# Optimization experiments

Hardware: AMD Instinct MI355X
Metric: run time of the kernel (lower is better)

Reference implementation:

```python
import jax, jax.numpy as jnp
import numpy as np


def _gcn_norm(edge_index, n_nodes):
    # add self-loops, compute symmetric normalization coeffs (PyG gcn_norm)
    loop = jnp.arange(n_nodes, dtype=edge_index.dtype)
    src = jnp.concatenate([edge_index[0], loop])
    dst = jnp.concatenate([edge_index[1], loop])
    ones = jnp.ones(src.shape[0], dtype=jnp.float32)
    deg = jax.ops.segment_sum(ones, dst, num_segments=n_nodes)
    dinv = jnp.where(deg > 0, jax.lax.rsqrt(deg), 0.0)
    norm = dinv[src] * dinv[dst]  # (E + n_nodes,)
    return src, dst, norm


def _gcn_conv(x, W, b, src, dst, norm, n_nodes):
    h = x @ W                                   # (N, C_out) small dense GEMM first (PyG order)
    msg = h[src] * norm[:, None]                # gather + normalize
    out = jax.ops.segment_sum(msg, dst, num_segments=n_nodes)  # scatter-add aggregate
    return out + b


def setup_inputs() -> dict:
    key = jax.random.key(0)
    k1, k2, k3, k4, k5, k6 = jax.random.split(key, 6)
    n_nodes, n_edges = 100000, 1600000
    in_c, hid_c, out_c = 4, 32, 16
    x = jax.random.normal(k1, (n_nodes, in_c), dtype=jnp.float32)
    edge_index = jax.random.randint(k2, (2, n_edges), 0, n_nodes, dtype=jnp.int64)
    # Glorot init like PyG GCNConv.lin, zero bias
    s1 = float(np.sqrt(6.0 / (in_c + hid_c)))
    s2 = float(np.sqrt(6.0 / (hid_c + out_c)))
    W1 = jax.random.uniform(k3, (in_c, hid_c), jnp.float32, -s1, s1)
    b1 = jnp.zeros((hid_c,), jnp.float32)
    W2 = jax.random.uniform(k4, (hid_c, out_c), jnp.float32, -s2, s2)
    b2 = jnp.zeros((out_c,), jnp.float32)
    return {"x": x, "edge_index": edge_index, "W1": W1, "b1": b1, "W2": W2, "b2": b2}


def reference(x, edge_index, W1, b1, W2, b2):
    n_nodes = x.shape[0]
    src, dst, norm = _gcn_norm(edge_index, n_nodes)
    h = _gcn_conv(x, W1, b1, src, dst, norm, n_nodes)
    h = jax.nn.relu(h)
    # dropout is identity in eval mode
    z = _gcn_conv(h, W2, b2, src, dst, norm, n_nodes)
    return z
```

## Files before the change

kernel.cpp:

```cpp
#include <hip/hip_runtime.h>

constexpr int HID = 32;
constexpr int OUTC = 16;
constexpr int BIN = 256;
constexpr int BSH = 8;
constexpr int MAXNB = 1024;
constexpr int PTILE = 2048;

typedef int iv4 __attribute__((ext_vector_type(4)));

static __device__ __forceinline__ float4 ld4(const float* p) { return *(const float4*)p; }

__global__ void k_zero(int* __restrict__ bcnt) {
    bcnt[threadIdx.x] = 0;
}

__global__ void k_part(const int* __restrict__ src, const int* __restrict__ dst,
                       int* __restrict__ bcnt, int* __restrict__ elist,
                       int E, int nb, int capb) {
    __shared__ int hist[MAXNB];
    __shared__ int base[MAXNB];
    const int t = threadIdx.x;
    for (int i = t; i < nb; i += blockDim.x) hist[i] = 0;
    __syncthreads();
    const int E4 = E >> 2;
    int d[8], s[8], r[8];
    bool val[2];
#pragma unroll
    for (int q = 0; q < 2; ++q) {
        const int v = blockIdx.x * (PTILE / 4) + q * 256 + t;
        val[q] = (v < E4);
        if (val[q]) {
            iv4 d4 = __builtin_nontemporal_load(((const iv4*)dst) + v);
            iv4 s4 = __builtin_nontemporal_load(((const iv4*)src) + v);
            d[q*4+0] = d4.x; d[q*4+1] = d4.y; d[q*4+2] = d4.z; d[q*4+3] = d4.w;
            s[q*4+0] = s4.x; s[q*4+1] = s4.y; s[q*4+2] = s4.z; s[q*4+3] = s4.w;
#pragma unroll
            for (int k = q*4; k < q*4+4; ++k) r[k] = atomicAdd(&hist[d[k] >> BSH], 1);
        }
    }
    __syncthreads();
    for (int i = t; i < nb; i += blockDim.x) {
        int h = hist[i];
        base[i] = h ? atomicAdd(&bcnt[i], h) : 0;
    }
    __syncthreads();
#pragma unroll
    for (int q = 0; q < 2; ++q) {
        if (val[q]) {
#pragma unroll
            for (int k = q*4; k < q*4+4; ++k) {
                int bin = d[k] >> BSH;
                int pos = base[bin] + r[k];
                if (pos < capb) elist[(size_t)bin * capb + pos] = (s[k] << BSH) | (d[k] & (BIN-1));
            }
        }
    }
    if (blockIdx.x == 0 && t < (E & 3)) {
        int j = (E4 << 2) + t;
        int dd = dst[j], ss = src[j];
        int bin = dd >> BSH;
        int pos = atomicAdd(&bcnt[bin], 1);
        if (pos < capb) elist[(size_t)bin * capb + pos] = (ss << BSH) | (dd & (BIN-1));
    }
}

__global__ void k_fill3(const int* __restrict__ elist, const int* __restrict__ bcnt,
                        int* __restrict__ cursor, int* __restrict__ eidx,
                        const float* __restrict__ x, float* __restrict__ dinv,
                        float* __restrict__ y, int capb, int CAP, int N) {
    __shared__ int cnt[BIN];
    const int b = blockIdx.x;
    const int bin0 = b << BSH;
    const int tid = threadIdx.x;
    if (tid < BIN) cnt[tid] = 0;
    __syncthreads();
    const int ecnt = min(bcnt[b], capb);
    const int* lst = elist + (size_t)b * capb;
    for (int i0 = tid * 4; i0 + 3 < ecnt; i0 += blockDim.x * 4) {
        iv4 e = *(const iv4*)(lst + i0);
        int l0 = e.x & (BIN-1), s0 = (unsigned)e.x >> BSH;
        int l1 = e.y & (BIN-1), s1 = (unsigned)e.y >> BSH;
        int l2 = e.z & (BIN-1), s2 = (unsigned)e.z >> BSH;
        int l3 = e.w & (BIN-1), s3 = (unsigned)e.w >> BSH;
        int p0 = atomicAdd(&cnt[l0], 1);
        int p1 = atomicAdd(&cnt[l1], 1);
        int p2 = atomicAdd(&cnt[l2], 1);
        int p3 = atomicAdd(&cnt[l3], 1);
        if (p0 < CAP) eidx[(size_t)(bin0 + l0) * CAP + p0] = s0;
        if (p1 < CAP) eidx[(size_t)(bin0 + l1) * CAP + p1] = s1;
        if (p2 < CAP) eidx[(size_t)(bin0 + l2) * CAP + p2] = s2;
        if (p3 < CAP) eidx[(size_t)(bin0 + l3) * CAP + p3] = s3;
    }
    const int tb = ecnt & ~3;
    if (tid < (ecnt & 3)) {
        int e = lst[tb + tid];
        int l = e & (BIN-1);
        int pos = atomicAdd(&cnt[l], 1);
        if (pos < CAP) eidx[(size_t)(bin0 + l) * CAP + pos] = (unsigned)e >> BSH;
    }
    __syncthreads();
    const int node = bin0 + tid;
    if (tid < BIN && node < N) {
        int deg = cnt[tid];
        cursor[node] = deg;
        float di = 1.0f / sqrtf((float)(deg + 1));
        dinv[node] = di;
        float4 xv = ld4(x + (size_t)node * 4);
        float4 yv; yv.x = xv.x * di; yv.y = xv.y * di; yv.z = xv.z * di; yv.w = xv.w * di;
        *(float4*)(y + (size_t)node * 4) = yv;
    }
}

__global__ void __launch_bounds__(64) k_layer1(
        const int* __restrict__ eidx, const int* __restrict__ degv,
        const float* __restrict__ dinv, const float* __restrict__ y,
        const float* __restrict__ W1, const float* __restrict__ b1,
        const float* __restrict__ W2, float* __restrict__ z, int N, int CAP) {
    __shared__ float sW1[4 * HID];
    __shared__ float sb1[HID];
    __shared__ float sW2[HID * OUTC];
    const int tid = threadIdx.x;
    for (int i = tid; i < 4 * HID; i += blockDim.x) sW1[i] = W1[i];
    for (int i = tid; i < HID; i += blockDim.x) sb1[i] = b1[i];
    for (int i = tid; i < HID * OUTC; i += blockDim.x) sW2[i] = W2[i];
    __syncthreads();
    const int n = blockIdx.x * blockDim.x + tid;
    if (n >= N) return;
    const int deg = min(degv[n], CAP);
    const int* bucket = eidx + (size_t)n * CAP;
    float4 a0 = {0,0,0,0}, a1 = {0,0,0,0}, a2 = {0,0,0,0}, a3 = {0,0,0,0};
    int i = 0;
    for (; i + 7 < deg; i += 8) {
        iv4 q0 = *(const iv4*)(bucket + i);
        iv4 q1 = *(const iv4*)(bucket + i + 4);
        float4 y0 = ld4(y + (size_t)q0.x * 4);
        float4 y1 = ld4(y + (size_t)q0.y * 4);
        float4 y2 = ld4(y + (size_t)q0.z * 4);
        float4 y3 = ld4(y + (size_t)q0.w * 4);
        float4 y4 = ld4(y + (size_t)q1.x * 4);
        float4 y5 = ld4(y + (size_t)q1.y * 4);
        float4 y6 = ld4(y + (size_t)q1.z * 4);
        float4 y7 = ld4(y + (size_t)q1.w * 4);
        a0.x += y0.x + y4.x; a0.y += y0.y + y4.y; a0.z += y0.z + y4.z; a0.w += y0.w + y4.w;
        a1.x += y1.x + y5.x; a1.y += y1.y + y5.y; a1.z += y1.z + y5.z; a1.w += y1.w + y5.w;
        a2.x += y2.x + y6.x; a2.y += y2.y + y6.y; a2.z += y2.z + y6.z; a2.w += y2.w + y6.w;
        a3.x += y3.x + y7.x; a3.y += y3.y + y7.y; a3.z += y3.z + y7.z; a3.w += y3.w + y7.w;
    }
    for (; i + 3 < deg; i += 4) {
        iv4 q0 = *(const iv4*)(bucket + i);
        float4 y0 = ld4(y + (size_t)q0.x * 4);
        float4 y1 = ld4(y + (size_t)q0.y * 4);
        float4 y2 = ld4(y + (size_t)q0.z * 4);
        float4 y3 = ld4(y + (size_t)q0.w * 4);
        a0.x += y0.x; a0.y += y0.y; a0.z += y0.z; a0.w += y0.w;
        a1.x += y1.x; a1.y += y1.y; a1.z += y1.z; a1.w += y1.w;
        a2.x += y2.x; a2.y += y2.y; a2.z += y2.z; a2.w += y2.w;
        a3.x += y3.x; a3.y += y3.y; a3.z += y3.z; a3.w += y3.w;
    }
    for (; i < deg; ++i) {
        float4 yv = ld4(y + (size_t)bucket[i] * 4);
        a0.x += yv.x; a0.y += yv.y; a0.z += yv.z; a0.w += yv.w;
    }
    const float di = dinv[n];
    float4 yn = ld4(y + (size_t)n * 4);
    float4 sv;
    sv.x = ((a0.x + a1.x) + (a2.x + a3.x) + yn.x) * di;
    sv.y = ((a0.y + a1.y) + (a2.y + a3.y) + yn.y) * di;
    sv.z = ((a0.z + a1.z) + (a2.z + a3.z) + yn.z) * di;
    sv.w = ((a0.w + a1.w) + (a2.w + a3.w) + yn.w) * di;
    float r[HID];
#pragma unroll
    for (int c = 0; c < HID; ++c)
        r[c] = fmaxf(sv.x * sW1[c] + sv.y * sW1[HID + c] +
                     sv.z * sW1[2*HID + c] + sv.w * sW1[3*HID + c] + sb1[c], 0.f);
    float o[OUTC] = {};
#pragma unroll
    for (int k = 0; k < HID; ++k)
#pragma unroll
        for (int c = 0; c < OUTC; ++c) o[c] += r[k] * sW2[k * OUTC + c];
    float* op = z + (size_t)n * OUTC;
#pragma unroll
    for (int c = 0; c < OUTC; c += 4) {
        float4 v;
        v.x = o[c] * di; v.y = o[c+1] * di; v.z = o[c+2] * di; v.w = o[c+3] * di;
        *(float4*)(op + c) = v;
    }
}

__global__ void k_agg2(const int* __restrict__ eidx, const int* __restrict__ degv,
                       const float* __restrict__ dinv, const float* __restrict__ z,
                       const float* __restrict__ b2, float* __restrict__ out,
                       int N, int CAP) {
    __shared__ float sb[OUTC];
    if (threadIdx.x < OUTC) sb[threadIdx.x] = b2[threadIdx.x];
    __syncthreads();
    const int tid = threadIdx.x;
    const int l4 = (tid & 3) * 4;
    const int n = blockIdx.x * (blockDim.x >> 2) + (tid >> 2);
    if (n >= N) return;
    const int deg = min(degv[n], CAP);
    const int* bucket = eidx + (size_t)n * CAP;
    float4 acc = {0,0,0,0}, acc2 = {0,0,0,0};
    int i = 0;
    for (; i + 7 < deg; i += 8) {
        iv4 q0 = *(const iv4*)(bucket + i);
        iv4 q1 = *(const iv4*)(bucket + i + 4);
        float4 r0 = ld4(z + (size_t)q0.x * OUTC + l4);
        float4 r1 = ld4(z + (size_t)q0.y * OUTC + l4);
        float4 r2 = ld4(z + (size_t)q0.z * OUTC + l4);
        float4 r3 = ld4(z + (size_t)q0.w * OUTC + l4);
        float4 r4 = ld4(z + (size_t)q1.x * OUTC + l4);
        float4 r5 = ld4(z + (size_t)q1.y * OUTC + l4);
        float4 r6 = ld4(z + (size_t)q1.z * OUTC + l4);
        float4 r7 = ld4(z + (size_t)q1.w * OUTC + l4);
        acc.x += r0.x + r1.x; acc.y += r0.y + r1.y; acc.z += r0.z + r1.z; acc.w += r0.w + r1.w;
        acc2.x += r2.x + r3.x; acc2.y += r2.y + r3.y; acc2.z += r2.z + r3.z; acc2.w += r2.w + r3.w;
        acc.x += r4.x + r5.x; acc.y += r4.y + r5.y; acc.z += r4.z + r5.z; acc.w += r4.w + r5.w;
        acc2.x += r6.x + r7.x; acc2.y += r6.y + r7.y; acc2.z += r6.z + r7.z; acc2.w += r6.w + r7.w;
    }
    for (; i + 3 < deg; i += 4) {
        iv4 q0 = *(const iv4*)(bucket + i);
        float4 r0 = ld4(z + (size_t)q0.x * OUTC + l4);
        float4 r1 = ld4(z + (size_t)q0.y * OUTC + l4);
        float4 r2 = ld4(z + (size_t)q0.z * OUTC + l4);
        float4 r3 = ld4(z + (size_t)q0.w * OUTC + l4);
        acc.x += r0.x + r1.x; acc.y += r0.y + r1.y; acc.z += r0.z + r1.z; acc.w += r0.w + r1.w;
        acc2.x += r2.x + r3.x; acc2.y += r2.y + r3.y; acc2.z += r2.z + r3.z; acc2.w += r2.w + r3.w;
    }
    for (; i < deg; ++i) {
        float4 r = ld4(z + (size_t)bucket[i] * OUTC + l4);
        acc.x += r.x; acc.y += r.y; acc.z += r.z; acc.w += r.w;
    }
    const float di = dinv[n];
    float4 zn = ld4(z + (size_t)n * OUTC + l4);
    float4 o;
    o.x = (acc.x + acc2.x + zn.x) * di + sb[l4 + 0];
    o.y = (acc.y + acc2.y + zn.y) * di + sb[l4 + 1];
    o.z = (acc.z + acc2.z + zn.z) * di + sb[l4 + 2];
    o.w = (acc.w + acc2.w + zn.w) * di + sb[l4 + 3];
    *(float4*)(out + (size_t)n * OUTC + l4) = o;
}

extern "C" void kernel_launch(void* const* d_in, const int* in_sizes, int n_in,
                              void* d_out, int out_size, void* d_ws, size_t ws_size,
                              hipStream_t stream) {
    const float* x  = (const float*)d_in[0];
    const int*   ei = (const int*)d_in[1];
    const float* W1 = (const float*)d_in[2];
    const float* b1 = (const float*)d_in[3];
    const float* W2 = (const float*)d_in[4];
    const float* b2 = (const float*)d_in[5];

    const int N = in_sizes[0] / 4;
    const int E = in_sizes[1] / 2;
    const int* src = ei;
    const int* dst = ei + E;

    const int nb = (N + BIN - 1) >> BSH;

    auto align = [](size_t v) { return (v + 255) & ~(size_t)255; };
    int capb = (E / nb + 1024 + 3) & ~3;
    int CAP = 64;
    auto total = [&](int cap, int cb) {
        return align((size_t)N * 4) + align((size_t)MAXNB * 4) + align((size_t)N * 4) +
               align((size_t)N * 4 * 4) + align((size_t)N * OUTC * 4) +
               align((size_t)N * cap * 4) + align((size_t)nb * (size_t)cb * 4);
    };
    while (capb > E / nb + 128 && total(CAP, capb) > ws_size) capb -= 256;
    while (CAP > 40 && total(CAP, capb) > ws_size) CAP -= 8;

    char* ws = (char*)d_ws;
    size_t off = 0;
    int*   cursor = (int*)(ws + off);   off += align((size_t)N * 4);
    int*   bcnt   = (int*)(ws + off);   off += align((size_t)MAXNB * 4);
    float* dinv   = (float*)(ws + off); off += align((size_t)N * 4);
    float* y      = (float*)(ws + off); off += align((size_t)N * 4 * 4);
    float* z      = (float*)(ws + off); off += align((size_t)N * OUTC * 4);
    int*   eidx   = (int*)(ws + off);   off += align((size_t)N * CAP * 4);
    int*   elist  = (int*)(ws + off);   off += align((size_t)nb * (size_t)capb * 4);
    (void)n_in;

    k_zero<<<1, MAXNB, 0, stream>>>(bcnt);
    k_part<<<(E + PTILE - 1) / PTILE, 256, 0, stream>>>(src, dst, bcnt, elist, E, nb, capb);
    k_fill3<<<nb, 512, 0, stream>>>(elist, bcnt, cursor, eidx, x, dinv, y, capb, CAP, N);
    k_layer1<<<(N + 63) / 64, 64, 0, stream>>>(eidx, cursor, dinv, y, W1, b1, W2, z, N, CAP);
    k_agg2<<<(N + 63) / 64, 256, 0, stream>>>(eidx, cursor, dinv, z, b2, (float*)d_out, N, CAP);
    (void)out_size;
}
```

Measured before the change: 94.62 us.

## Split layer-1 node aggregation across four lanes with shuffle reduction

The layer-1 kernel now gives each node four threads instead of one. The lanes stride the neighbour bucket in interleaved chunks of four and combine their partial sums with xor shuffles. Each lane then computes one quarter of the 16 output channels of the second weight multiply and writes one float4. This spreads the irregular per-node gather over more threads, which helps hide latency and balance degree variation, and it cuts per-thread register use. The cost is that every lane redundantly computes the 32-wide hidden activation.

```diff
diff --git a/kernel.cpp b/kernel.cpp
--- a/kernel.cpp
+++ b/kernel.cpp
@@ -112,7 +112,7 @@
     }
 }
 
-__global__ void __launch_bounds__(64) k_layer1(
+__global__ void __launch_bounds__(256) k_layer1(
         const int* __restrict__ eidx, const int* __restrict__ degv,
         const float* __restrict__ dinv, const float* __restrict__ y,
         const float* __restrict__ W1, const float* __restrict__ b1,
@@ -121,71 +121,59 @@
     __shared__ float sb1[HID];
     __shared__ float sW2[HID * OUTC];
     const int tid = threadIdx.x;
-    for (int i = tid; i < 4 * HID; i += blockDim.x) sW1[i] = W1[i];
-    for (int i = tid; i < HID; i += blockDim.x) sb1[i] = b1[i];
+    if (tid < 4 * HID) sW1[tid] = W1[tid];
+    if (tid < HID) sb1[tid] = b1[tid];
     for (int i = tid; i < HID * OUTC; i += blockDim.x) sW2[i] = W2[i];
     __syncthreads();
-    const int n = blockIdx.x * blockDim.x + tid;
+    const int g = tid & 3;
+    const int n = blockIdx.x * (blockDim.x >> 2) + (tid >> 2);
     if (n >= N) return;
     const int deg = min(degv[n], CAP);
     const int* bucket = eidx + (size_t)n * CAP;
-    float4 a0 = {0,0,0,0}, a1 = {0,0,0,0}, a2 = {0,0,0,0}, a3 = {0,0,0,0};
-    int i = 0;
-    for (; i + 7 < deg; i += 8) {
-        iv4 q0 = *(const iv4*)(bucket + i);
-        iv4 q1 = *(const iv4*)(bucket + i + 4);
-        float4 y0 = ld4(y + (size_t)q0.x * 4);
-        float4 y1 = ld4(y + (size_t)q0.y * 4);
-        float4 y2 = ld4(y + (size_t)q0.z * 4);
-        float4 y3 = ld4(y + (size_t)q0.w * 4);
-        float4 y4 = ld4(y + (size_t)q1.x * 4);
-        float4 y5 = ld4(y + (size_t)q1.y * 4);
-        float4 y6 = ld4(y + (size_t)q1.z * 4);
-        float4 y7 = ld4(y + (size_t)q1.w * 4);
-        a0.x += y0.x + y4.x; a0.y += y0.y + y4.y; a0.z += y0.z + y4.z; a0.w += y0.w + y4.w;
-        a1.x += y1.x + y5.x; a1.y += y1.y + y5.y; a1.z += y1.z + y5.z; a1.w += y1.w + y5.w;
-        a2.x += y2.x + y6.x; a2.y += y2.y + y6.y; a2.z += y2.z + y6.z; a2.w += y2.w + y6.w;
-        a3.x += y3.x + y7.x; a3.y += y3.y + y7.y; a3.z += y3.z + y7.z; a3.w += y3.w + y7.w;
-    }
-    for (; i + 3 < deg; i += 4) {
-        iv4 q0 = *(const iv4*)(bucket + i);
-        float4 y0 = ld4(y + (size_t)q0.x * 4);
-        float4 y1 = ld4(y + (size_t)q0.y * 4);
-        float4 y2 = ld4(y + (size_t)q0.z * 4);
-        float4 y3 = ld4(y + (size_t)q0.w * 4);
-        a0.x += y0.x; a0.y += y0.y; a0.z += y0.z; a0.w += y0.w;
-        a1.x += y1.x; a1.y += y1.y; a1.z += y1.z; a1.w += y1.w;
-        a2.x += y2.x; a2.y += y2.y; a2.z += y2.z; a2.w += y2.w;
-        a3.x += y3.x; a3.y += y3.y; a3.z += y3.z; a3.w += y3.w;
-    }
-    for (; i < deg; ++i) {
-        float4 yv = ld4(y + (size_t)bucket[i] * 4);
-        a0.x += yv.x; a0.y += yv.y; a0.z += yv.z; a0.w += yv.w;
-    }
+    float4 a = {0,0,0,0};
+    for (int base = g * 4; base + 3 < deg; base += 16) {
+        iv4 q = *(const iv4*)(bucket + base);
+        float4 y0 = ld4(y + (size_t)q.x * 4);
+        float4 y1 = ld4(y + (size_t)q.y * 4);
+        float4 y2 = ld4(y + (size_t)q.z * 4);
+        float4 y3 = ld4(y + (size_t)q.w * 4);
+        a.x += (y0.x + y1.x) + (y2.x + y3.x);
+        a.y += (y0.y + y1.y) + (y2.y + y3.y);
+        a.z += (y0.z + y1.z) + (y2.z + y3.z);
+        a.w += (y0.w + y1.w) + (y2.w + y3.w);
+    }
+    const int tb = deg & ~3;
+    if (g < (deg & 3)) {
+        float4 yv = ld4(y + (size_t)bucket[tb + g] * 4);
+        a.x += yv.x; a.y += yv.y; a.z += yv.z; a.w += yv.w;
+    }
+    a.x += __shfl_xor(a.x, 1); a.y += __shfl_xor(a.y, 1);
+    a.z += __shfl_xor(a.z, 1); a.w += __shfl_xor(a.w, 1);
+    a.x += __shfl_xor(a.x, 2); a.y += __shfl_xor(a.y, 2);
+    a.z += __shfl_xor(a.z, 2); a.w += __shfl_xor(a.w, 2);
+
     const float di = dinv[n];
     float4 yn = ld4(y + (size_t)n * 4);
     float4 sv;
-    sv.x = ((a0.x + a1.x) + (a2.x + a3.x) + yn.x) * di;
-    sv.y = ((a0.y + a1.y) + (a2.y + a3.y) + yn.y) * di;
-    sv.z = ((a0.z + a1.z) + (a2.z + a3.z) + yn.z) * di;
-    sv.w = ((a0.w + a1.w) + (a2.w + a3.w) + yn.w) * di;
+    sv.x = (a.x + yn.x) * di;
+    sv.y = (a.y + yn.y) * di;
+    sv.z = (a.z + yn.z) * di;
+    sv.w = (a.w + yn.w) * di;
     float r[HID];
 #pragma unroll
     for (int c = 0; c < HID; ++c)
         r[c] = fmaxf(sv.x * sW1[c] + sv.y * sW1[HID + c] +
                      sv.z * sW1[2*HID + c] + sv.w * sW1[3*HID + c] + sb1[c], 0.f);
-    float o[OUTC] = {};
-#pragma unroll
-    for (int k = 0; k < HID; ++k)
-#pragma unroll
-        for (int c = 0; c < OUTC; ++c) o[c] += r[k] * sW2[k * OUTC + c];
-    float* op = z + (size_t)n * OUTC;
-#pragma unroll
-    for (int c = 0; c < OUTC; c += 4) {
-        float4 v;
-        v.x = o[c] * di; v.y = o[c+1] * di; v.z = o[c+2] * di; v.w = o[c+3] * di;
-        *(float4*)(op + c) = v;
-    }
+    float o[4] = {};
+#pragma unroll
+    for (int k = 0; k < HID; ++k) {
+        const float rk = r[k];
+#pragma unroll
+        for (int c = 0; c < 4; ++c) o[c] += rk * sW2[k * OUTC + g * 4 + c];
+    }
+    float4 v;
+    v.x = o[0] * di; v.y = o[1] * di; v.z = o[2] * di; v.w = o[3] * di;
+    *(float4*)(z + (size_t)n * OUTC + g * 4) = v;
 }
 
 __global__ void k_agg2(const int* __restrict__ eidx, const int* __restrict__ degv,
@@ -284,7 +272,7 @@
     k_zero<<<1, MAXNB, 0, stream>>>(bcnt);
     k_part<<<(E + PTILE - 1) / PTILE, 256, 0, stream>>>(src, dst, bcnt, elist, E, nb, capb);
     k_fill3<<<nb, 512, 0, stream>>>(elist, bcnt, cursor, eidx, x, dinv, y, capb, CAP, N);
-    k_layer1<<<(N + 63) / 64, 64, 0, stream>>>(eidx, cursor, dinv, y, W1, b1, W2, z, N, CAP);
+    k_layer1<<<(N + 63) / 64, 256, 0, stream>>>(eidx, cursor, dinv, y, W1, b1, W2, z, N, CAP);
     k_agg2<<<(N + 63) / 64, 256, 0, stream>>>(eidx, cursor, dinv, z, b2, (float*)d_out, N, CAP);
     (void)out_size;
 }
```

Result: no change. 93.66 us (-1.0%).
